# Performance work log

Measured on AMD Instinct MI355X. Metric: run time of the kernel, lower is better.

The kernel has to match this reference:

```python
import jax, jax.numpy as jnp
import numpy as np

B, S, D, H = 4, 2048, 1024, 16
HD = D // H

def setup_inputs() -> dict:
    key = jax.random.key(0)
    ks = jax.random.split(key, 5)
    x = jax.random.normal(ks[0], (B, S, D), dtype=jnp.float32)
    mask = jnp.ones((B, S), dtype=jnp.int32)
    # torch nn.Linear init scale ~ 1/sqrt(fan_in); use small normal for stability
    qkv_w = jax.random.normal(ks[1], (3 * D, D), dtype=jnp.float32) * (1.0 / np.sqrt(D))
    qkv_b = jax.random.normal(ks[2], (3 * D,), dtype=jnp.float32) * 0.02
    out_w = jax.random.normal(ks[3], (D, D), dtype=jnp.float32) * (1.0 / np.sqrt(D))
    out_b = jax.random.normal(ks[4], (D,), dtype=jnp.float32) * 0.02
    return {"x": x, "mask": mask, "qkv_w": qkv_w, "qkv_b": qkv_b,
            "out_w": out_w, "out_b": out_b}

def reference(x, mask, qkv_w, qkv_b, out_w, out_b):
    b, s, d = x.shape
    scale = np.sqrt(HD).astype(np.float32)
    # qkv projection: torch Linear y = x @ W^T + b
    qkv = x @ qkv_w.T + qkv_b                      # (b, s, 3d)
    qkv = qkv.reshape(b, s, 3, H, HD)
    qkv = jnp.transpose(qkv, (2, 0, 3, 1, 4))      # (3, b, H, s, hd)
    q, k, v = qkv[0], qkv[1], qkv[2]
    scores = jnp.einsum('bhqd,bhkd->bhqk', q, k) / scale  # (b, H, s, s)
    neg_inf = jnp.float32(-jnp.inf)
    causal = jnp.tril(jnp.ones((s, s), dtype=bool))
    scores = jnp.where(causal[None, None], scores, neg_inf)
    key_mask = (mask != 0)[:, None, None, :]       # (b, 1, 1, s)
    scores = jnp.where(key_mask, scores, neg_inf)
    attn = jax.nn.softmax(scores, axis=-1)
    out = jnp.einsum('bhqk,bhkd->bhqd', attn, v)   # (b, H, s, hd)
    out = jnp.transpose(out, (0, 2, 1, 3)).reshape(b, s, d)
    return out @ out_w.T + out_b
```

## Files before the change

kernel.cpp:

```cpp
#include <hip/hip_runtime.h>
#include <stdint.h>
#include <type_traits>

#define BB  4
#define SS  2048
#define DD  1024
#define HH  16
#define HDD 64

typedef __attribute__((ext_vector_type(8))) short s16x8;
typedef __attribute__((ext_vector_type(4))) float f32x4;

__device__ inline short f2bf(float f) {
    union { float f; unsigned int u; } v; v.f = f;
    unsigned int r = (v.u + 0x7fffu + ((v.u >> 16) & 1u)) >> 16;
    return (short)r;
}

__device__ inline float bf2f(short s) {
    union { unsigned int u; float f; } v;
    v.u = ((unsigned int)(unsigned short)s) << 16;
    return v.f;
}

#define GLL(gp, lp) __builtin_amdgcn_global_load_lds( \
    (const __attribute__((address_space(1))) void*)(gp), \
    (__attribute__((address_space(3))) void*)(lp), 16, 0, 0)

__device__ inline void lds_barrier() {
    asm volatile("s_waitcnt lgkmcnt(0)" ::: "memory");
    __builtin_amdgcn_sched_barrier(0);
    __builtin_amdgcn_s_barrier();
    __builtin_amdgcn_sched_barrier(0);
}

__global__ void cvt_kernel(const float* __restrict__ src, short* __restrict__ dst, int n) {
    int i = (blockIdx.x * 256 + threadIdx.x) * 8;
    if (i >= n) return;
    const float4* s = (const float4*)(src + i);
    float4 a = s[0], b = s[1];
    s16x8 o;
    o[0]=f2bf(a.x); o[1]=f2bf(a.y); o[2]=f2bf(a.z); o[3]=f2bf(a.w);
    o[4]=f2bf(b.x); o[5]=f2bf(b.y); o[6]=f2bf(b.z); o[7]=f2bf(b.w);
    *(s16x8*)(dst + i) = o;
}

template<int EPI>
__global__ __launch_bounds__(256, 2)
void gemm128(const short* __restrict__ A, const short* __restrict__ Bw,
             const float* __restrict__ bias, float* __restrict__ Cf,
             short* __restrict__ Qo, short* __restrict__ Ko, short* __restrict__ Vo,
             int M, int N, int K, int nbx)
{
    __shared__ short lsA[2][128 * 64];
    __shared__ short lsB[2][128 * 64];

    const int tid  = threadIdx.x;
    const int w    = tid >> 6, lane = tid & 63;
    const int quad = lane >> 4, l15 = lane & 15;
    const int wm = w >> 1, wn = w & 1;
    const int cpx = gridDim.x >> 3;
    const int swz = (blockIdx.x & 7) * cpx + (blockIdx.x >> 3);
    const int m0 = (swz / nbx) * 128, n0 = (swz % nbx) * 128;
    const int grow = lane >> 3;
    const int gcol = ((lane & 7) ^ grow) * 8;
    const int l7 = l15 & 7;

    f32x4 acc[4][4] = {};

    auto issue = [&](int kt, int buf) {
#pragma unroll
        for (int jj = 0; jj < 4; ++jj) {
            int row = w * 32 + jj * 8 + grow;
            GLL(A + (size_t)(m0 + row) * K + kt * 64 + gcol,
                &lsA[buf][(w * 4 + jj) * 512]);
        }
#pragma unroll
        for (int jj = 0; jj < 4; ++jj) {
            int row = w * 32 + jj * 8 + grow;
            GLL(Bw + (size_t)(n0 + row) * K + kt * 64 + gcol,
                &lsB[buf][(w * 4 + jj) * 512]);
        }
    };

    const int NT = K >> 6;
    issue(0, 0);
    for (int t = 0; t < NT; ++t) {
        const int buf = t & 1;
        lds_barrier();
        if (t + 1 < NT) {
            issue(t + 1, buf ^ 1);
            asm volatile("s_waitcnt vmcnt(8)" ::: "memory");
        } else {
            asm volatile("s_waitcnt vmcnt(0)" ::: "memory");
        }
        __builtin_amdgcn_sched_barrier(0);
        __builtin_amdgcn_s_barrier();
        __builtin_amdgcn_sched_barrier(0);

        s16x8 af[4][2], bfr[4][2];
#pragma unroll
        for (int mf = 0; mf < 4; ++mf)
#pragma unroll
            for (int ks = 0; ks < 2; ++ks)
                af[mf][ks] = *(const s16x8*)&lsA[buf][(wm * 64 + mf * 16 + l15) * 64 +
                                                     (((ks * 4 + quad) ^ l7) * 8)];
#pragma unroll
        for (int nf = 0; nf < 4; ++nf)
#pragma unroll
            for (int ks = 0; ks < 2; ++ks)
                bfr[nf][ks] = *(const s16x8*)&lsB[buf][(wn * 64 + nf * 16 + l15) * 64 +
                                                      (((ks * 4 + quad) ^ l7) * 8)];

        __builtin_amdgcn_s_setprio(1);
#pragma unroll
        for (int ks = 0; ks < 2; ++ks)
#pragma unroll
            for (int mf = 0; mf < 4; ++mf)
#pragma unroll
                for (int nf = 0; nf < 4; ++nf)
                    acc[mf][nf] = __builtin_amdgcn_mfma_f32_16x16x32_bf16(
                                      af[mf][ks], bfr[nf][ks], acc[mf][nf], 0, 0, 0);
        __builtin_amdgcn_s_setprio(0);
    }

    if (EPI == 0) {
#pragma unroll
        for (int mf = 0; mf < 4; ++mf) {
            int row = m0 + wm * 64 + mf * 16 + quad * 4;
#pragma unroll
            for (int nf = 0; nf < 4; ++nf) {
                int col = n0 + wn * 64 + nf * 16 + l15;
                float bv = bias[col];
#pragma unroll
                for (int r = 0; r < 4; ++r)
                    Cf[(size_t)(row + r) * N + col] = acc[mf][nf][r] + bv;
            }
        }
    } else {
#pragma unroll
        for (int mf = 0; mf < 4; ++mf) {
            int row = m0 + wm * 64 + mf * 16 + quad * 4;
#pragma unroll
            for (int nf = 0; nf < 4; ++nf) {
                int col = n0 + wn * 64 + nf * 16 + l15;
                float bv = bias[col];
                int sel = col >> 10, h = (col >> 6) & 15, hd = col & 63;
#pragma unroll
                for (int r = 0; r < 4; ++r) {
                    int rr = row + r;
                    int b = rr >> 11, s = rr & 2047;
                    short val = f2bf(acc[mf][nf][r] + bv);
                    if (sel == 0)      Qo[(((size_t)b * HH + h) * SS + s) * HDD + hd] = val;
                    else if (sel == 1) Ko[(((size_t)b * HH + h) * SS + s) * HDD + hd] = val;
                    else               Vo[(((size_t)b * HH + h) * HDD + hd) * SS + s] = val;
                }
            }
        }
    }
}

__global__ __launch_bounds__(256, 2)
void attn_kernel(const short* __restrict__ Q, const short* __restrict__ Kb,
                 const short* __restrict__ Vb, const int* __restrict__ mask,
                 short* __restrict__ O)
{
    __shared__ short lsK[2][64 * 64];
    __shared__ short lsV[2][64 * 64];
    __shared__ short lsP[4][32 * 64];
    __shared__ short lsM[SS];

    const int tid  = threadIdx.x;
    const int w    = tid >> 6, lane = tid & 63;
    const int quad = lane >> 4, l15 = lane & 15;
    const int bx = blockIdx.x, bh = blockIdx.y;
    const int b = bh >> 4;
    const size_t baseQK = (size_t)bh * SS * HDD;
    const size_t baseV  = (size_t)bh * HDD * SS;
    const float SC = 0.18033688f;
    const int grow = lane >> 3;
    const int gcol = ((lane & 7) ^ grow) * 8;
    const int l7 = l15 & 7;

    {
        const int4* mp = (const int4*)(mask + b * SS);
        int4 a = mp[tid * 2], c = mp[tid * 2 + 1];
        const short NEG = f2bf(-1e30f);
        s16x8 mo;
        mo[0] = a.x ? (short)0 : NEG; mo[1] = a.y ? (short)0 : NEG;
        mo[2] = a.z ? (short)0 : NEG; mo[3] = a.w ? (short)0 : NEG;
        mo[4] = c.x ? (short)0 : NEG; mo[5] = c.y ? (short)0 : NEG;
        mo[6] = c.z ? (short)0 : NEG; mo[7] = c.w ? (short)0 : NEG;
        *(s16x8*)&lsM[tid * 8] = mo;
    }

    auto issue = [&](int kv0, int buf) {
#pragma unroll
        for (int jj = 0; jj < 2; ++jj) {
            int row = w * 16 + jj * 8 + grow;
            GLL(Kb + baseQK + (size_t)(kv0 + row) * HDD + gcol,
                &lsK[buf][(w * 2 + jj) * 512]);
        }
#pragma unroll
        for (int jj = 0; jj < 2; ++jj) {
            int row = w * 16 + jj * 8 + grow;
            GLL(Vb + baseV + (size_t)row * SS + kv0 + gcol,
                &lsV[buf][(w * 2 + jj) * 512]);
        }
    };

    for (int t = 0; t < 2; ++t) {
        const int qb = t ? bx : (15 - bx);
        const int q0 = qb * 128;
        const int qw0 = q0 + w * 32;

        s16x8 aq[2][2];
#pragma unroll
        for (int s = 0; s < 2; ++s)
#pragma unroll
            for (int ks = 0; ks < 2; ++ks)
                aq[s][ks] = *(const s16x8*)(Q + baseQK +
                    (size_t)(qw0 + s * 16 + l15) * HDD + ks * 32 + quad * 8);

        float m_r[2][4], l_r[2][4];
        f32x4 o_acc[2][4] = {};
#pragma unroll
        for (int s = 0; s < 2; ++s)
#pragma unroll
            for (int r = 0; r < 4; ++r) { m_r[s][r] = -1e30f; l_r[s][r] = 0.f; }

        const int ntiles = 2 * qb + 2;

        lds_barrier();
        issue(0, 0);

        auto tile = [&](auto CC, int kv0, int buf, int kvn) {
            constexpr bool CAUS = decltype(CC)::value;

            lds_barrier();
            if (kvn >= 0) issue(kvn, buf ^ 1);

            float madd[4];
#pragma unroll
            for (int nt = 0; nt < 4; ++nt)
                madd[nt] = bf2f(lsM[kv0 + nt * 16 + l15]);

            if (kvn >= 0) asm volatile("s_waitcnt vmcnt(4)" ::: "memory");
            else          asm volatile("s_waitcnt vmcnt(0)" ::: "memory");
            __builtin_amdgcn_sched_barrier(0);
            __builtin_amdgcn_s_barrier();
            __builtin_amdgcn_sched_barrier(0);

            f32x4 sv[2][4];
#pragma unroll
            for (int s = 0; s < 2; ++s)
#pragma unroll
                for (int nt = 0; nt < 4; ++nt) sv[s][nt] = f32x4{};
#pragma unroll
            for (int ks = 0; ks < 2; ++ks)
#pragma unroll
                for (int nt = 0; nt < 4; ++nt) {
                    s16x8 kf = *(const s16x8*)&lsK[buf][(nt * 16 + l15) * 64 +
                                                       (((ks * 4 + quad) ^ l7) * 8)];
#pragma unroll
                    for (int s = 0; s < 2; ++s)
                        sv[s][nt] = __builtin_amdgcn_mfma_f32_16x16x32_bf16(
                                        aq[s][ks], kf, sv[s][nt], 0, 0, 0);
                }

#pragma unroll
            for (int s = 0; s < 2; ++s) {
                const int rowg0 = qw0 + s * 16 + quad * 4;
#pragma unroll
                for (int nt = 0; nt < 4; ++nt) {
                    int colg = kv0 + nt * 16 + l15;
#pragma unroll
                    for (int r = 0; r < 4; ++r) {
                        float scv = sv[s][nt][r] * SC + madd[nt];
                        if (CAUS && colg > rowg0 + r) scv = -1e30f;
                        sv[s][nt][r] = scv;
                    }
                }
            }

            float rm[2][4];
#pragma unroll
            for (int s = 0; s < 2; ++s)
#pragma unroll
                for (int r = 0; r < 4; ++r) {
                    float v = fmaxf(fmaxf(sv[s][0][r], sv[s][1][r]),
                                    fmaxf(sv[s][2][r], sv[s][3][r]));
                    v = fmaxf(v, __shfl_xor(v, 1));
                    v = fmaxf(v, __shfl_xor(v, 2));
                    v = fmaxf(v, __shfl_xor(v, 4));
                    v = fmaxf(v, __shfl_xor(v, 8));
                    rm[s][r] = v;
                }
            float need = rm[0][0] - m_r[0][0];
#pragma unroll
            for (int s = 0; s < 2; ++s)
#pragma unroll
                for (int r = 0; r < 4; ++r)
                    need = fmaxf(need, rm[s][r] - m_r[s][r]);
            if (!__all(need <= 8.0f)) {
#pragma unroll
                for (int s = 0; s < 2; ++s)
#pragma unroll
                    for (int r = 0; r < 4; ++r) {
                        float nm = fmaxf(m_r[s][r], rm[s][r]);
                        float al = __builtin_amdgcn_exp2f(m_r[s][r] - nm);
                        m_r[s][r] = nm;
                        l_r[s][r] *= al;
#pragma unroll
                        for (int ht = 0; ht < 4; ++ht)
                            o_acc[s][ht][r] *= al;
                    }
            }
#pragma unroll
            for (int s = 0; s < 2; ++s)
#pragma unroll
                for (int r = 0; r < 4; ++r) {
                    float rs = 0.f;
#pragma unroll
                    for (int nt = 0; nt < 4; ++nt) {
                        float p = __builtin_amdgcn_exp2f(sv[s][nt][r] - m_r[s][r]);
                        sv[s][nt][r] = p;
                        rs += p;
                    }
                    l_r[s][r] += rs;
                }

            short* lsPw = lsP[w];
#pragma unroll
            for (int s = 0; s < 2; ++s)
#pragma unroll
                for (int nt = 0; nt < 4; ++nt)
#pragma unroll
                    for (int r = 0; r < 4; ++r) {
                        int prow = s * 16 + quad * 4 + r;
                        lsPw[prow * 64 + (((nt * 2 + (l15 >> 3)) ^ (prow & 7)) << 3) + l7]
                            = f2bf(sv[s][nt][r]);
                    }
            asm volatile("s_waitcnt lgkmcnt(0)" ::: "memory");
            __builtin_amdgcn_sched_barrier(0);

            s16x8 ap[2][2];
#pragma unroll
            for (int s = 0; s < 2; ++s)
#pragma unroll
                for (int k2 = 0; k2 < 2; ++k2)
                    ap[s][k2] = *(const s16x8*)&lsPw[(s * 16 + l15) * 64 +
                                                     (((k2 * 4 + quad) ^ l7) << 3)];
#pragma unroll
            for (int ht = 0; ht < 4; ++ht)
#pragma unroll
                for (int k2 = 0; k2 < 2; ++k2) {
                    s16x8 vf = *(const s16x8*)&lsV[buf][(ht * 16 + l15) * 64 +
                                                        (((k2 * 4 + quad) ^ l7) * 8)];
#pragma unroll
                    for (int s = 0; s < 2; ++s)
                        o_acc[s][ht] = __builtin_amdgcn_mfma_f32_16x16x32_bf16(
                                           ap[s][k2], vf, o_acc[s][ht], 0, 0, 0);
                }
        };

        for (int kt = 0; kt < ntiles; ++kt) {
            const int kvn = (kt + 1 < ntiles) ? (kt + 1) * 64 : -1;
            if (kt >= 2 * qb) tile(std::true_type{},  kt * 64, kt & 1, kvn);
            else              tile(std::false_type{}, kt * 64, kt & 1, kvn);
        }

        const int hcol = (bh & 15) * HDD;
#pragma unroll
        for (int s = 0; s < 2; ++s)
#pragma unroll
            for (int r = 0; r < 4; ++r) {
                float ls = l_r[s][r];
                ls += __shfl_xor(ls, 1);
                ls += __shfl_xor(ls, 2);
                ls += __shfl_xor(ls, 4);
                ls += __shfl_xor(ls, 8);
                float inv = 1.0f / ls;
                int srow = qw0 + s * 16 + quad * 4 + r;
                size_t base = ((size_t)b * SS + srow) * DD + hcol;
#pragma unroll
                for (int ht = 0; ht < 4; ++ht)
                    O[base + ht * 16 + l15] = f2bf(o_acc[s][ht][r] * inv);
            }
    }
}

extern "C" void kernel_launch(void* const* d_in, const int* in_sizes, int n_in,
                              void* d_out, int out_size, void* d_ws, size_t ws_size,
                              hipStream_t stream) {
    const float* x     = (const float*)d_in[0];
    const int*   mask  = (const int*)d_in[1];
    const float* qkv_w = (const float*)d_in[2];
    const float* qkv_b = (const float*)d_in[3];
    const float* out_w = (const float*)d_in[4];
    const float* out_b = (const float*)d_in[5];
    float* out = (float*)d_out;

    const size_t M1 = (size_t)BB * SS;
    short* ws  = (short*)d_ws;
    short* xb  = ws;
    short* qwb = xb  + M1 * DD;
    short* owb = qwb + (size_t)3 * DD * DD;
    short* Qb  = owb + (size_t)DD * DD;
    short* Kb  = Qb  + M1 * DD;
    short* Vb  = Kb  + M1 * DD;
    short* Ob  = Vb  + M1 * DD;

    cvt_kernel<<<(int)(M1 * DD / 8 / 256), 256, 0, stream>>>(x, xb, (int)(M1 * DD));
    cvt_kernel<<<3 * DD * DD / 8 / 256, 256, 0, stream>>>(qkv_w, qwb, 3 * DD * DD);
    cvt_kernel<<<DD * DD / 8 / 256, 256, 0, stream>>>(out_w, owb, DD * DD);

    gemm128<1><<<1536, 256, 0, stream>>>(xb, qwb, qkv_b, nullptr,
                                         Qb, Kb, Vb, 8192, 3072, 1024, 24);
    attn_kernel<<<dim3(8, BB * HH), 256, 0, stream>>>(Qb, Kb, Vb, mask, Ob);
    gemm128<0><<<512, 256, 0, stream>>>(Ob, owb, out_b, out,
                                        nullptr, nullptr, nullptr, 8192, 1024, 1024, 8);
}
```

Baseline: 308.4 us.

## Software-pipeline QK^T of next tile with softmax and PV of current tile

Restructures the flash-attention inner loop so the QK^T MFMAs for tile t+1 are issued before the P·V MFMAs of tile t, and splits K and V prefetch so K is loaded two tiles ahead and V one tile ahead. The aim is to overlap the softmax VALU work and global-load latency with matrix-core work instead of serialising them per tile. The causal mask changes from a compile-time template branch to a runtime flag, and an extra set of score registers is kept live, which raises register pressure and may lower occupancy.

```diff
diff --git a/kernel.cpp b/kernel.cpp
--- a/kernel.cpp
+++ b/kernel.cpp
@@ -194,13 +194,15 @@
         *(s16x8*)&lsM[tid * 8] = mo;
     }
 
-    auto issue = [&](int kv0, int buf) {
+    auto issueK = [&](int kv0, int buf) {
 #pragma unroll
         for (int jj = 0; jj < 2; ++jj) {
             int row = w * 16 + jj * 8 + grow;
             GLL(Kb + baseQK + (size_t)(kv0 + row) * HDD + gcol,
                 &lsK[buf][(w * 2 + jj) * 512]);
         }
+    };
+    auto issueV = [&](int kv0, int buf) {
 #pragma unroll
         for (int jj = 0; jj < 2; ++jj) {
             int row = w * 16 + jj * 8 + grow;
@@ -209,8 +211,8 @@
         }
     };
 
-    for (int t = 0; t < 2; ++t) {
-        const int qb = t ? bx : (15 - bx);
+    for (int t2 = 0; t2 < 2; ++t2) {
+        const int qb = t2 ? bx : (15 - bx);
         const int q0 = qb * 128;
         const int qw0 = q0 + w * 32;
 
@@ -229,45 +231,48 @@
 #pragma unroll
             for (int r = 0; r < 4; ++r) { m_r[s][r] = -1e30f; l_r[s][r] = 0.f; }
 
-        const int ntiles = 2 * qb + 2;
+        const int n = 2 * qb + 2;
+
+        auto qkt = [&](int kbuf, f32x4 (&svo)[2][4]) {
+#pragma unroll
+            for (int s = 0; s < 2; ++s)
+#pragma unroll
+                for (int nt = 0; nt < 4; ++nt) svo[s][nt] = f32x4{};
+#pragma unroll
+            for (int ks = 0; ks < 2; ++ks)
+#pragma unroll
+                for (int nt = 0; nt < 4; ++nt) {
+                    s16x8 kf = *(const s16x8*)&lsK[kbuf][(nt * 16 + l15) * 64 +
+                                                        (((ks * 4 + quad) ^ l7) * 8)];
+#pragma unroll
+                    for (int s = 0; s < 2; ++s)
+                        svo[s][nt] = __builtin_amdgcn_mfma_f32_16x16x32_bf16(
+                                         aq[s][ks], kf, svo[s][nt], 0, 0, 0);
+                }
+        };
 
         lds_barrier();
-        issue(0, 0);
-
-        auto tile = [&](auto CC, int kv0, int buf, int kvn) {
-            constexpr bool CAUS = decltype(CC)::value;
-
+        issueK(0, 0); issueV(0, 0); issueK(64, 1);
+        asm volatile("s_waitcnt vmcnt(2)" ::: "memory");
+        __builtin_amdgcn_sched_barrier(0);
+        __builtin_amdgcn_s_barrier();
+        __builtin_amdgcn_sched_barrier(0);
+
+        f32x4 sv[2][4];
+        qkt(0, sv);
+
+        for (int t = 0; t < n; ++t) {
+            const int buf = t & 1;
             lds_barrier();
-            if (kvn >= 0) issue(kvn, buf ^ 1);
-
+            if (t + 2 < n) issueK((t + 2) * 64, buf);
+            if (t + 1 < n) issueV((t + 1) * 64, buf ^ 1);
+
+            const bool caus = (t >= n - 2);
+            const int kv0 = t * 64;
             float madd[4];
 #pragma unroll
             for (int nt = 0; nt < 4; ++nt)
                 madd[nt] = bf2f(lsM[kv0 + nt * 16 + l15]);
-
-            if (kvn >= 0) asm volatile("s_waitcnt vmcnt(4)" ::: "memory");
-            else          asm volatile("s_waitcnt vmcnt(0)" ::: "memory");
-            __builtin_amdgcn_sched_barrier(0);
-            __builtin_amdgcn_s_barrier();
-            __builtin_amdgcn_sched_barrier(0);
-
-            f32x4 sv[2][4];
-#pragma unroll
-            for (int s = 0; s < 2; ++s)
-#pragma unroll
-                for (int nt = 0; nt < 4; ++nt) sv[s][nt] = f32x4{};
-#pragma unroll
-            for (int ks = 0; ks < 2; ++ks)
-#pragma unroll
-                for (int nt = 0; nt < 4; ++nt) {
-                    s16x8 kf = *(const s16x8*)&lsK[buf][(nt * 16 + l15) * 64 +
-                                                       (((ks * 4 + quad) ^ l7) * 8)];
-#pragma unroll
-                    for (int s = 0; s < 2; ++s)
-                        sv[s][nt] = __builtin_amdgcn_mfma_f32_16x16x32_bf16(
-                                        aq[s][ks], kf, sv[s][nt], 0, 0, 0);
-                }
-
 #pragma unroll
             for (int s = 0; s < 2; ++s) {
                 const int rowg0 = qw0 + s * 16 + quad * 4;
@@ -277,12 +282,11 @@
 #pragma unroll
                     for (int r = 0; r < 4; ++r) {
                         float scv = sv[s][nt][r] * SC + madd[nt];
-                        if (CAUS && colg > rowg0 + r) scv = -1e30f;
+                        if (caus && colg > rowg0 + r) scv = -1e30f;
                         sv[s][nt][r] = scv;
                     }
                 }
             }
-
             float rm[2][4];
 #pragma unroll
             for (int s = 0; s < 2; ++s)
@@ -330,6 +334,17 @@
                     l_r[s][r] += rs;
                 }
 
+            __builtin_amdgcn_sched_barrier(0);
+            if (t + 2 < n)      asm volatile("s_waitcnt vmcnt(4)" ::: "memory");
+            else if (t + 1 < n) asm volatile("s_waitcnt vmcnt(2)" ::: "memory");
+            else                asm volatile("s_waitcnt vmcnt(0)" ::: "memory");
+            __builtin_amdgcn_sched_barrier(0);
+            __builtin_amdgcn_s_barrier();
+            __builtin_amdgcn_sched_barrier(0);
+
+            f32x4 svn[2][4];
+            if (t + 1 < n) qkt(buf ^ 1, svn);
+
             short* lsPw = lsP[w];
 #pragma unroll
             for (int s = 0; s < 2; ++s)
@@ -362,12 +377,14 @@
                         o_acc[s][ht] = __builtin_amdgcn_mfma_f32_16x16x32_bf16(
                                            ap[s][k2], vf, o_acc[s][ht], 0, 0, 0);
                 }
-        };
-
-        for (int kt = 0; kt < ntiles; ++kt) {
-            const int kvn = (kt + 1 < ntiles) ? (kt + 1) * 64 : -1;
-            if (kt >= 2 * qb) tile(std::true_type{},  kt * 64, kt & 1, kvn);
-            else              tile(std::false_type{}, kt * 64, kt & 1, kvn);
+
+            if (t + 1 < n) {
+#pragma unroll
+                for (int s = 0; s < 2; ++s)
+#pragma unroll
+                    for (int nt = 0; nt < 4; ++nt)
+                        sv[s][nt] = svn[s][nt];
+            }
         }
 
         const int hcol = (bh & 15) * HDD;
```

Result: no change. 314.6 us (+2.0%).

## Transpose QK^T MFMA so each lane owns a query row in softmax

Applied to the files above, without the earlier changes.

Swaps the MFMA operands for the score computation so the S tile comes out transposed: each lane holds one query row across four key columns. Row max and sum then reduce mostly within a lane, needing two cross-lane shuffles instead of four per row, and per-lane softmax state shrinks from 8 to 2 values. P is written to LDS as packed 64-bit stores instead of scalar bf16 stores. The cost is extra __shfl calls to redistribute the rescale factors and normalizers back to the accumulator layout.

```diff
diff --git a/kernel.cpp b/kernel.cpp
--- a/kernel.cpp
+++ b/kernel.cpp
@@ -21,6 +21,11 @@
     union { unsigned int u; float f; } v;
     v.u = ((unsigned int)(unsigned short)s) << 16;
     return v.f;
+}
+
+__device__ inline unsigned int pk2(float a, float b) {
+    return (unsigned int)(unsigned short)f2bf(a) |
+           ((unsigned int)(unsigned short)f2bf(b) << 16);
 }
 
 #define GLL(gp, lp) __builtin_amdgcn_global_load_lds( \
@@ -222,12 +227,10 @@
                 aq[s][ks] = *(const s16x8*)(Q + baseQK +
                     (size_t)(qw0 + s * 16 + l15) * HDD + ks * 32 + quad * 8);
 
-        float m_r[2][4], l_r[2][4];
+        float m_r[2], l_r[2];
         f32x4 o_acc[2][4] = {};
 #pragma unroll
-        for (int s = 0; s < 2; ++s)
-#pragma unroll
-            for (int r = 0; r < 4; ++r) { m_r[s][r] = -1e30f; l_r[s][r] = 0.f; }
+        for (int s = 0; s < 2; ++s) { m_r[s] = -1e30f; l_r[s] = 0.f; }
 
         const int ntiles = 2 * qb + 2;
 
@@ -240,10 +243,15 @@
             lds_barrier();
             if (kvn >= 0) issue(kvn, buf ^ 1);
 
-            float madd[4];
-#pragma unroll
-            for (int nt = 0; nt < 4; ++nt)
-                madd[nt] = bf2f(lsM[kv0 + nt * 16 + l15]);
+            float madd[4][4];
+#pragma unroll
+            for (int nt = 0; nt < 4; ++nt) {
+                uint2 mw4 = *(const uint2*)&lsM[kv0 + nt * 16 + quad * 4];
+                madd[nt][0] = bf2f((short)(mw4.x & 0xffff));
+                madd[nt][1] = bf2f((short)(mw4.x >> 16));
+                madd[nt][2] = bf2f((short)(mw4.y & 0xffff));
+                madd[nt][3] = bf2f((short)(mw4.y >> 16));
+            }
 
             if (kvn >= 0) asm volatile("s_waitcnt vmcnt(4)" ::: "memory");
             else          asm volatile("s_waitcnt vmcnt(0)" ::: "memory");
@@ -265,82 +273,83 @@
 #pragma unroll
                     for (int s = 0; s < 2; ++s)
                         sv[s][nt] = __builtin_amdgcn_mfma_f32_16x16x32_bf16(
-                                        aq[s][ks], kf, sv[s][nt], 0, 0, 0);
+                                        kf, aq[s][ks], sv[s][nt], 0, 0, 0);
                 }
 
 #pragma unroll
             for (int s = 0; s < 2; ++s) {
-                const int rowg0 = qw0 + s * 16 + quad * 4;
+                const int qg = qw0 + s * 16 + l15;
 #pragma unroll
                 for (int nt = 0; nt < 4; ++nt) {
-                    int colg = kv0 + nt * 16 + l15;
+                    const int kg0 = kv0 + nt * 16 + quad * 4;
 #pragma unroll
                     for (int r = 0; r < 4; ++r) {
-                        float scv = sv[s][nt][r] * SC + madd[nt];
-                        if (CAUS && colg > rowg0 + r) scv = -1e30f;
+                        float scv = sv[s][nt][r] * SC + madd[nt][r];
+                        if (CAUS && kg0 + r > qg) scv = -1e30f;
                         sv[s][nt][r] = scv;
                     }
                 }
             }
 
-            float rm[2][4];
-#pragma unroll
-            for (int s = 0; s < 2; ++s)
-#pragma unroll
-                for (int r = 0; r < 4; ++r) {
-                    float v = fmaxf(fmaxf(sv[s][0][r], sv[s][1][r]),
-                                    fmaxf(sv[s][2][r], sv[s][3][r]));
-                    v = fmaxf(v, __shfl_xor(v, 1));
-                    v = fmaxf(v, __shfl_xor(v, 2));
-                    v = fmaxf(v, __shfl_xor(v, 4));
-                    v = fmaxf(v, __shfl_xor(v, 8));
-                    rm[s][r] = v;
-                }
-            float need = rm[0][0] - m_r[0][0];
-#pragma unroll
-            for (int s = 0; s < 2; ++s)
-#pragma unroll
-                for (int r = 0; r < 4; ++r)
-                    need = fmaxf(need, rm[s][r] - m_r[s][r]);
+            float rm[2];
+#pragma unroll
+            for (int s = 0; s < 2; ++s) {
+                float v = fmaxf(fmaxf(fmaxf(sv[s][0][0], sv[s][0][1]),
+                                      fmaxf(sv[s][0][2], sv[s][0][3])),
+                                fmaxf(fmaxf(sv[s][1][0], sv[s][1][1]),
+                                      fmaxf(sv[s][1][2], sv[s][1][3])));
+                float v2 = fmaxf(fmaxf(fmaxf(sv[s][2][0], sv[s][2][1]),
+                                       fmaxf(sv[s][2][2], sv[s][2][3])),
+                                 fmaxf(fmaxf(sv[s][3][0], sv[s][3][1]),
+                                       fmaxf(sv[s][3][2], sv[s][3][3])));
+                v = fmaxf(v, v2);
+                v = fmaxf(v, __shfl_xor(v, 16));
+                v = fmaxf(v, __shfl_xor(v, 32));
+                rm[s] = v;
+            }
+            float need = fmaxf(rm[0] - m_r[0], rm[1] - m_r[1]);
             if (!__all(need <= 8.0f)) {
 #pragma unroll
-                for (int s = 0; s < 2; ++s)
+                for (int s = 0; s < 2; ++s) {
+                    float nm = fmaxf(m_r[s], rm[s]);
+                    float al = __builtin_amdgcn_exp2f(m_r[s] - nm);
+                    m_r[s] = nm;
+                    l_r[s] *= al;
 #pragma unroll
                     for (int r = 0; r < 4; ++r) {
-                        float nm = fmaxf(m_r[s][r], rm[s][r]);
-                        float al = __builtin_amdgcn_exp2f(m_r[s][r] - nm);
-                        m_r[s][r] = nm;
-                        l_r[s][r] *= al;
+                        float alq = __shfl(al, (quad << 2) + r + (lane & 48));
 #pragma unroll
                         for (int ht = 0; ht < 4; ++ht)
-                            o_acc[s][ht][r] *= al;
+                            o_acc[s][ht][r] *= alq;
                     }
-            }
-#pragma unroll
-            for (int s = 0; s < 2; ++s)
-#pragma unroll
-                for (int r = 0; r < 4; ++r) {
-                    float rs = 0.f;
-#pragma unroll
-                    for (int nt = 0; nt < 4; ++nt) {
-                        float p = __builtin_amdgcn_exp2f(sv[s][nt][r] - m_r[s][r]);
+                }
+            }
+#pragma unroll
+            for (int s = 0; s < 2; ++s) {
+                float rs = 0.f;
+#pragma unroll
+                for (int nt = 0; nt < 4; ++nt)
+#pragma unroll
+                    for (int r = 0; r < 4; ++r) {
+                        float p = __builtin_amdgcn_exp2f(sv[s][nt][r] - m_r[s]);
                         sv[s][nt][r] = p;
                         rs += p;
                     }
-                    l_r[s][r] += rs;
-                }
+                l_r[s] += rs;
+            }
 
             short* lsPw = lsP[w];
 #pragma unroll
             for (int s = 0; s < 2; ++s)
 #pragma unroll
-                for (int nt = 0; nt < 4; ++nt)
-#pragma unroll
-                    for (int r = 0; r < 4; ++r) {
-                        int prow = s * 16 + quad * 4 + r;
-                        lsPw[prow * 64 + (((nt * 2 + (l15 >> 3)) ^ (prow & 7)) << 3) + l7]
-                            = f2bf(sv[s][nt][r]);
-                    }
+                for (int nt = 0; nt < 4; ++nt) {
+                    uint2 pw;
+                    pw.x = pk2(sv[s][nt][0], sv[s][nt][1]);
+                    pw.y = pk2(sv[s][nt][2], sv[s][nt][3]);
+                    int row = s * 16 + l15;
+                    int g8 = (nt * 2 + (quad >> 1)) ^ l7;
+                    *(uint2*)&lsPw[row * 64 + (g8 << 3) + ((quad & 1) << 2)] = pw;
+                }
             asm volatile("s_waitcnt lgkmcnt(0)" ::: "memory");
             __builtin_amdgcn_sched_barrier(0);
 
@@ -372,21 +381,21 @@
 
         const int hcol = (bh & 15) * HDD;
 #pragma unroll
-        for (int s = 0; s < 2; ++s)
+        for (int s = 0; s < 2; ++s) {
+            float ls = l_r[s];
+            ls += __shfl_xor(ls, 16);
+            ls += __shfl_xor(ls, 32);
 #pragma unroll
             for (int r = 0; r < 4; ++r) {
-                float ls = l_r[s][r];
-                ls += __shfl_xor(ls, 1);
-                ls += __shfl_xor(ls, 2);
-                ls += __shfl_xor(ls, 4);
-                ls += __shfl_xor(ls, 8);
-                float inv = 1.0f / ls;
+                float lq = __shfl(ls, (quad << 2) + r + (lane & 48));
+                float inv = 1.0f / lq;
                 int srow = qw0 + s * 16 + quad * 4 + r;
                 size_t base = ((size_t)b * SS + srow) * DD + hcol;
 #pragma unroll
                 for (int ht = 0; ht < 4; ++ht)
                     O[base + ht * 16 + l15] = f2bf(o_acc[s][ht][r] * inv);
             }
+        }
     }
 }
 
```

Result: faster. 292.1 us (-5.3%).
